# Kernel tuning notes

Hardware: AMD Instinct MI355X
Metric: run time of the kernel (lower is better)

Reference implementation:

```python
import jax, jax.numpy as jnp
import numpy as np

DIM = 192
HEADS = 6
WIN = (2, 6, 2)
N_TOK = WIN[0] * WIN[1] * WIN[2]  # 24
MLP_HID = 4 * DIM


def _rel_pos_index():
    wh, ww, wd = WIN
    ch, cw, cd = np.meshgrid(np.arange(wh), np.arange(ww), np.arange(wd), indexing='ij')
    coords = np.stack([ch, cw, cd]).reshape(3, -1)  # (3, N)
    rel = coords[:, :, None] - coords[:, None, :]   # (3, N, N)
    rel = rel.transpose(1, 2, 0).copy()
    rel[:, :, 0] += wh - 1
    rel[:, :, 1] += ww - 1
    rel[:, :, 2] += wd - 1
    rel[:, :, 0] *= (2 * ww - 1) * (2 * wd - 1)
    rel[:, :, 1] *= 2 * wd - 1
    return rel.sum(-1)  # (N, N) int


def setup_inputs() -> dict:
    key = jax.random.key(0)
    ks = jax.random.split(key, 8)
    wh, ww, wd = WIN
    table_len = (2 * wh - 1) * (2 * ww - 1) * (2 * wd - 1)
    return {
        'x': jax.random.normal(ks[0], (2, 48, 96, 14, DIM), jnp.float32),
        'ln1_g': jnp.ones((DIM,), jnp.float32),
        'ln1_b': jnp.zeros((DIM,), jnp.float32),
        'qkv_w': jax.random.normal(ks[1], (DIM, 3 * DIM), jnp.float32) * 0.02,  # [in, out]
        'qkv_b': jnp.zeros((3 * DIM,), jnp.float32),
        'bias_table': jax.random.normal(ks[2], (table_len, HEADS), jnp.float32) * 0.02,
        'proj_w': jax.random.normal(ks[3], (DIM, DIM), jnp.float32) * 0.02,
        'proj_b': jnp.zeros((DIM,), jnp.float32),
        'ln2_g': jnp.ones((DIM,), jnp.float32),
        'ln2_b': jnp.zeros((DIM,), jnp.float32),
        'mlp_w1': jax.random.normal(ks[4], (DIM, MLP_HID), jnp.float32) * 0.02,
        'mlp_b1': jnp.zeros((MLP_HID,), jnp.float32),
        'mlp_w2': jax.random.normal(ks[5], (MLP_HID, DIM), jnp.float32) * 0.02,
        'mlp_b2': jnp.zeros((DIM,), jnp.float32),
        'rel_index': jnp.asarray(_rel_pos_index(), jnp.int32),  # (N, N)
    }


def _layernorm(x, g, b, eps=1e-5):
    mu = jnp.mean(x, -1, keepdims=True)
    var = jnp.mean(jnp.square(x - mu), -1, keepdims=True)
    return (x - mu) * jax.lax.rsqrt(var + eps) * g + b


def reference(x, ln1_g, ln1_b, qkv_w, qkv_b, bias_table, proj_w, proj_b,
              ln2_g, ln2_b, mlp_w1, mlp_b1, mlp_w2, mlp_b2, rel_index):
    B, H, W, D, C = x.shape
    wh, ww, wd = WIN
    pad_h, pad_w, pad_d = (-H) % wh, (-W) % ww, (-D) % wd
    if pad_h or pad_w or pad_d:
        x = jnp.pad(x, ((0, 0), (0, pad_h), (0, pad_w), (0, pad_d), (0, 0)))
    Hp, Wp, Dp = H + pad_h, W + pad_w, D + pad_d
    # window partition -> (num_windows*B, N, C)
    xw = x.reshape(B, Hp // wh, wh, Wp // ww, ww, Dp // wd, wd, C)
    xw = xw.transpose(0, 1, 3, 5, 2, 4, 6, 7).reshape(-1, N_TOK, C)
    shortcut = xw

    h = _layernorm(xw, ln1_g, ln1_b)
    qkv = (h @ qkv_w + qkv_b).reshape(-1, N_TOK, 3, HEADS, C // HEADS)
    q, k, v = qkv[:, :, 0], qkv[:, :, 1], qkv[:, :, 2]  # (Bw, N, H, hd)
    scale = (C // HEADS) ** -0.5
    attn = jnp.einsum('bnhd,bmhd->bhnm', q * scale, k)
    bias = bias_table[rel_index]  # (N, N, HEADS)
    attn = attn + bias.transpose(2, 0, 1)[None]
    attn = jax.nn.softmax(attn, axis=-1)
    out = jnp.einsum('bhnm,bmhd->bnhd', attn, v).reshape(-1, N_TOK, C)
    out = out @ proj_w + proj_b
    xw = shortcut + out

    h2 = _layernorm(xw, ln2_g, ln2_b)
    mlp = jax.nn.gelu(h2 @ mlp_w1 + mlp_b1, approximate=False) @ mlp_w2 + mlp_b2
    xw = xw + mlp

    # reverse window partition
    xw = xw.reshape(B, Hp // wh, Wp // ww, Dp // wd, wh, ww, wd, C)
    xw = xw.transpose(0, 1, 4, 2, 5, 3, 6, 7).reshape(B, Hp, Wp, Dp, C)
    if pad_h or pad_w or pad_d:
        xw = xw[:, :H, :W, :D, :]
    return xw
```

## Files before the change

kernel.cpp:

```cpp
#include <hip/hip_runtime.h>
#include <hip/hip_bf16.h>
#include <math.h>

typedef __bf16 bf16_t;
typedef __bf16 bf16x8 __attribute__((ext_vector_type(8)));
typedef float  f32x4  __attribute__((ext_vector_type(4)));

#define NBLK 2688
#define WP_QKV  0
#define WP_PROJ 55296
#define WP_MLP1 73728
#define WP_MLP2 147456
#define WP_TOT  221184
#define WF_QKV  0
#define WF_PROJ 110592
#define WF_MLP1 147456
#define WF_MLP2 294912

__global__ void preproc_all(const float* __restrict__ qkv_w, const float* __restrict__ proj_w,
                            const float* __restrict__ mlp_w1, const float* __restrict__ mlp_w2,
                            bf16_t* __restrict__ dst) {
    int p = blockIdx.x * 256 + threadIdx.x;
    if (p >= WP_TOT) return;
    const float* W; int N, Kt; int q = p;
    if (p < WP_PROJ)      { W = qkv_w;  N = 576; Kt = 6;  }
    else if (p < WP_MLP1) { W = proj_w; N = 192; Kt = 6;  q -= WP_PROJ; }
    else if (p < WP_MLP2) { W = mlp_w1; N = 768; Kt = 6;  q -= WP_MLP1; }
    else                  { W = mlp_w2; N = 192; Kt = 24; q -= WP_MLP2; }
    int j    = (q & 3) * 2;
    int lane = (q >> 2) & 63;
    int kt   = (q >> 8) % Kt;
    int nt   = (q >> 8) / Kt;
    int k = kt * 32 + (lane >> 4) * 8 + j;
    int n = nt * 16 + (lane & 15);
    union { bf16_t h[2]; unsigned u; } pk;
    pk.h[0] = (bf16_t)W[k * N + n];
    pk.h[1] = (bf16_t)W[(k + 1) * N + n];
    *(unsigned*)(dst + p * 2) = pk.u;
}

__global__ __launch_bounds__(384, 3)
void pangu_main(const float* __restrict__ x,
                const float* __restrict__ ln1_g, const float* __restrict__ ln1_b,
                const float* __restrict__ qkv_b,
                const float* __restrict__ bias_table,
                const float* __restrict__ proj_b,
                const float* __restrict__ ln2_g, const float* __restrict__ ln2_b,
                const float* __restrict__ mlp_b1, const float* __restrict__ mlp_b2,
                const int* __restrict__ rel_index,
                const bf16_t* __restrict__ wf,
                float* __restrict__ out)
{
    __shared__ __align__(16) unsigned char arena[46080];
    __shared__ int   sRowOff[48];
    __shared__ float sMu[48], sRs[48];

    unsigned char* aAb   = arena;
    unsigned char* aOb   = arena;
    unsigned char* aH2b  = arena;
    unsigned char* xw2b  = arena + 19200;
    unsigned char* aHidb = arena + 19200;
    bf16_t* aO   = (bf16_t*)aOb;
    bf16_t* aHid = (bf16_t*)aHidb;
    bf16_t* xw2h = (bf16_t*)xw2b;

    const int t    = threadIdx.x;
    const int lane = t & 63;
    const int wv   = t >> 6;
    const int quad = lane >> 4;
    const int l15  = lane & 15;
    const int q4   = quad * 4;

    if (t < 48) {
        int win = t / 24, tok = t % 24;
        int W = blockIdx.x * 2 + win;
        int id_ = W % 7;  int r1 = W / 7;
        int iw_ = r1 % 16; int r2 = r1 / 16;
        int ih_ = r2 % 24; int b  = r2 / 24;
        int i = tok / 12, j = (tok % 12) / 2, k = tok % 2;
        sRowOff[t] = (((b * 48 + ih_ * 2 + i) * 96 + iw_ * 6 + j) * 14 + id_ * 2 + k) * 192;
    }
    __syncthreads();

    {
        int r48 = t >> 3, l = t & 7;
        const float* xr = x + sRowOff[r48];
        float4 v[6];
        #pragma unroll
        for (int s = 0; s < 6; ++s) v[s] = *(const float4*)(xr + l * 4 + s * 32);
        float sm = 0.f, s2 = 0.f;
        #pragma unroll
        for (int s = 0; s < 6; ++s) {
            sm += v[s].x + v[s].y + v[s].z + v[s].w;
            s2 += v[s].x * v[s].x + v[s].y * v[s].y + v[s].z * v[s].z + v[s].w * v[s].w;
        }
        sm += __shfl_xor(sm, 1); s2 += __shfl_xor(s2, 1);
        sm += __shfl_xor(sm, 2); s2 += __shfl_xor(s2, 2);
        sm += __shfl_xor(sm, 4); s2 += __shfl_xor(s2, 4);
        float mu = sm * (1.f / 192.f);
        float var = s2 * (1.f / 192.f) - mu * mu;
        float rs = rsqrtf(var + 1e-5f);
        int row = r48;
        #pragma unroll
        for (int s = 0; s < 6; ++s) {
            int c = l * 4 + s * 32;
            union { bf16_t h[4]; uint2 u; } pk;
            pk.h[0] = (bf16_t)((v[s].x - mu) * rs * ln1_g[c]     + ln1_b[c]);
            pk.h[1] = (bf16_t)((v[s].y - mu) * rs * ln1_g[c + 1] + ln1_b[c + 1]);
            pk.h[2] = (bf16_t)((v[s].z - mu) * rs * ln1_g[c + 2] + ln1_b[c + 2]);
            pk.h[3] = (bf16_t)((v[s].w - mu) * rs * ln1_g[c + 3] + ln1_b[c + 3]);
            *(uint2*)(aAb + row * 400 + c * 2) = pk.u;
        }
    }
    __syncthreads();

    {
        const int h = wv;
        unsigned char* wb = arena + 19200 + wv * 4480;
        bf16_t* Qb = (bf16_t*)wb;
        bf16_t* Kb = (bf16_t*)(wb + 1920);
        bf16_t* Vt = (bf16_t*)(wb + 1920);
        bf16_t* Pb = (bf16_t*)wb;

        f32x4 acc[3][6];
        {
            float bq[6];
            const int ntg[6] = {2*h, 2*h+1, 12+2*h, 13+2*h, 24+2*h, 25+2*h};
            #pragma unroll
            for (int n = 0; n < 6; ++n) bq[n] = qkv_b[ntg[n] * 16 + l15];
            #pragma unroll
            for (int m = 0; m < 3; ++m)
                #pragma unroll
                for (int n = 0; n < 6; ++n)
                    acc[m][n] = (f32x4){bq[n], bq[n], bq[n], bq[n]};
            for (int kt = 0; kt < 6; ++kt) {
                bf16x8 af[3];
                #pragma unroll
                for (int m = 0; m < 3; ++m)
                    af[m] = *(const bf16x8*)(aAb + (l15 + m * 16) * 400 + kt * 64 + quad * 16);
                #pragma unroll
                for (int n = 0; n < 6; ++n) {
                    bf16x8 bfr = *(const bf16x8*)(wf + WF_QKV + ((ntg[n] * 6 + kt) * 64 + lane) * 8);
                    #pragma unroll
                    for (int m = 0; m < 3; ++m)
                        acc[m][n] = __builtin_amdgcn_mfma_f32_16x16x32_bf16(af[m], bfr, acc[m][n], 0, 0, 0);
                }
            }
        }
        __syncthreads();

        const float scale = 0.1767766952966369f;
        #pragma unroll
        for (int win = 0; win < 2; ++win) {
            #pragma unroll
            for (int m = 0; m < 3; ++m)
                #pragma unroll
                for (int i = 0; i < 4; ++i) {
                    int tok = m * 16 + q4 + i - win * 24;
                    if (tok >= 0 && tok < 24) {
                        #pragma unroll
                        for (int nt = 0; nt < 2; ++nt) {
                            int d = nt * 16 + l15;
                            Qb[tok * 40 + d] = (bf16_t)(acc[m][nt][i] * scale);
                            Kb[tok * 40 + d] = (bf16_t)(acc[m][2+nt][i]);
                        }
                    }
                }
            f32x4 sacc[2][2];
            #pragma unroll
            for (int mt = 0; mt < 2; ++mt)
                #pragma unroll
                for (int nt = 0; nt < 2; ++nt)
                    #pragma unroll
                    for (int i = 0; i < 4; ++i) {
                        int n = mt * 16 + q4 + i; if (n > 23) n = 23;
                        int m = nt * 16 + l15;    if (m > 23) m = 23;
                        sacc[mt][nt][i] = bias_table[rel_index[n * 24 + m] * 6 + h];
                    }
            #pragma unroll
            for (int nt = 0; nt < 2; ++nt) {
                bf16x8 kf = *(const bf16x8*)((unsigned char*)Kb + (l15 + nt * 16) * 80 + quad * 16);
                #pragma unroll
                for (int mt = 0; mt < 2; ++mt) {
                    bf16x8 qf = *(const bf16x8*)((unsigned char*)Qb + (l15 + mt * 16) * 80 + quad * 16);
                    sacc[mt][nt] = __builtin_amdgcn_mfma_f32_16x16x32_bf16(qf, kf, sacc[mt][nt], 0, 0, 0);
                }
            }
            #pragma unroll
            for (int m = 0; m < 3; ++m)
                #pragma unroll
                for (int i = 0; i < 4; ++i) {
                    int tok = m * 16 + q4 + i - win * 24;
                    if (tok >= 0 && tok < 24) {
                        #pragma unroll
                        for (int nt = 0; nt < 2; ++nt)
                            Vt[(nt * 16 + l15) * 40 + tok] = (bf16_t)(acc[m][4+nt][i]);
                    }
                }
            {
                int d = lane >> 1, half = lane & 1;
                *(uint2*)((unsigned char*)Vt + d * 80 + 48 + half * 8) = make_uint2(0u, 0u);
            }
            #pragma unroll
            for (int mt = 0; mt < 2; ++mt)
                #pragma unroll
                for (int i = 0; i < 4; ++i) {
                    float s0 = sacc[mt][0][i];
                    float s1m = (l15 < 8) ? sacc[mt][1][i] : -1e30f;
                    float mx = fmaxf(s0, s1m);
                    mx = fmaxf(mx, __shfl_xor(mx, 1));
                    mx = fmaxf(mx, __shfl_xor(mx, 2));
                    mx = fmaxf(mx, __shfl_xor(mx, 4));
                    mx = fmaxf(mx, __shfl_xor(mx, 8));
                    float e0 = __expf(s0 - mx);
                    float e1 = (l15 < 8) ? __expf(sacc[mt][1][i] - mx) : 0.f;
                    float sum = e0 + e1;
                    sum += __shfl_xor(sum, 1);
                    sum += __shfl_xor(sum, 2);
                    sum += __shfl_xor(sum, 4);
                    sum += __shfl_xor(sum, 8);
                    float inv = 1.f / sum;
                    sacc[mt][0][i] = e0 * inv;
                    sacc[mt][1][i] = e1 * inv;
                }
            #pragma unroll
            for (int mt = 0; mt < 2; ++mt)
                #pragma unroll
                for (int i = 0; i < 4; ++i) {
                    int r = mt * 16 + q4 + i;
                    if (r < 24) {
                        Pb[r * 40 + l15]      = (bf16_t)sacc[mt][0][i];
                        Pb[r * 40 + 16 + l15] = (bf16_t)sacc[mt][1][i];
                    }
                }
            f32x4 oacc[2][2];
            #pragma unroll
            for (int mt = 0; mt < 2; ++mt)
                #pragma unroll
                for (int nt = 0; nt < 2; ++nt)
                    oacc[mt][nt] = (f32x4){0.f, 0.f, 0.f, 0.f};
            #pragma unroll
            for (int nt = 0; nt < 2; ++nt) {
                bf16x8 vf = *(const bf16x8*)((unsigned char*)Vt + (l15 + nt * 16) * 80 + quad * 16);
                #pragma unroll
                for (int mt = 0; mt < 2; ++mt) {
                    bf16x8 pf = *(const bf16x8*)((unsigned char*)Pb + (l15 + mt * 16) * 80 + quad * 16);
                    oacc[mt][nt] = __builtin_amdgcn_mfma_f32_16x16x32_bf16(pf, vf, oacc[mt][nt], 0, 0, 0);
                }
            }
            #pragma unroll
            for (int mt = 0; mt < 2; ++mt)
                #pragma unroll
                for (int i = 0; i < 4; ++i) {
                    int tok = mt * 16 + q4 + i;
                    if (tok < 24) {
                        int r = win * 24 + tok;
                        #pragma unroll
                        for (int nt = 0; nt < 2; ++nt)
                            aO[r * 200 + h * 32 + nt * 16 + l15] = (bf16_t)oacc[mt][nt][i];
                    }
                }
        }
    }
    __syncthreads();

    float rxw[3][2][4];
    {
        f32x4 pacc[3][2];
        #pragma unroll
        for (int m = 0; m < 3; ++m)
            #pragma unroll
            for (int n = 0; n < 2; ++n) pacc[m][n] = (f32x4){0.f, 0.f, 0.f, 0.f};
        for (int kt = 0; kt < 6; ++kt) {
            bf16x8 af[3];
            #pragma unroll
            for (int m = 0; m < 3; ++m)
                af[m] = *(const bf16x8*)(aOb + (l15 + m * 16) * 400 + kt * 64 + quad * 16);
            #pragma unroll
            for (int n = 0; n < 2; ++n) {
                int NT = wv * 2 + n;
                bf16x8 bfr = *(const bf16x8*)(wf + WF_PROJ + ((NT * 6 + kt) * 64 + lane) * 8);
                #pragma unroll
                for (int m = 0; m < 3; ++m)
                    pacc[m][n] = __builtin_amdgcn_mfma_f32_16x16x32_bf16(af[m], bfr, pacc[m][n], 0, 0, 0);
            }
        }
        __syncthreads();
        #pragma unroll
        for (int n = 0; n < 2; ++n) {
            int c = (wv * 2 + n) * 16 + l15;
            float pb = proj_b[c];
            #pragma unroll
            for (int m = 0; m < 3; ++m)
                #pragma unroll
                for (int i = 0; i < 4; ++i) {
                    int r = m * 16 + q4 + i;
                    float val = x[sRowOff[r] + c] + pb + pacc[m][n][i];
                    rxw[m][n][i] = val;
                    xw2h[r * 200 + c] = (bf16_t)val;
                }
        }
    }
    __syncthreads();

    {
        int r = t >> 3, l = t & 7;
        float sm = 0.f, s2 = 0.f;
        #pragma unroll
        for (int s = 0; s < 6; ++s) {
            union { bf16_t h[4]; uint2 u; } pk;
            pk.u = *(const uint2*)(xw2b + r * 400 + l * 8 + s * 64);
            #pragma unroll
            for (int z = 0; z < 4; ++z) { float v = (float)pk.h[z]; sm += v; s2 += v * v; }
        }
        sm += __shfl_xor(sm, 1); s2 += __shfl_xor(s2, 1);
        sm += __shfl_xor(sm, 2); s2 += __shfl_xor(s2, 2);
        sm += __shfl_xor(sm, 4); s2 += __shfl_xor(s2, 4);
        if (l == 0) {
            float mu = sm * (1.f / 192.f);
            float var = s2 * (1.f / 192.f) - mu * mu;
            sMu[r] = mu; sRs[r] = rsqrtf(var + 1e-5f);
        }
    }
    __syncthreads();
    for (int p = t; p < 4608; p += 384) {
        int r = p / 96, c2 = p % 96, c = c2 * 2;
        float mu = sMu[r], rs = sRs[r];
        union { bf16_t h[2]; unsigned u; } in, pk;
        in.u = *(const unsigned*)(xw2b + r * 400 + c2 * 4);
        pk.h[0] = (bf16_t)(((float)in.h[0] - mu) * rs * ln2_g[c]     + ln2_b[c]);
        pk.h[1] = (bf16_t)(((float)in.h[1] - mu) * rs * ln2_g[c + 1] + ln2_b[c + 1]);
        *(unsigned*)(aH2b + r * 400 + c2 * 4) = pk.u;
    }
    __syncthreads();

    f32x4 acc2[3][2];
    #pragma unroll
    for (int m = 0; m < 3; ++m)
        #pragma unroll
        for (int n = 0; n < 2; ++n) {
            float b2 = mlp_b2[(wv * 2 + n) * 16 + l15];
            acc2[m][n] = (f32x4){b2, b2, b2, b2};
        }
    for (int ch = 0; ch < 4; ++ch) {
        f32x4 a1[3][2];
        #pragma unroll
        for (int m = 0; m < 3; ++m)
            #pragma unroll
            for (int n = 0; n < 2; ++n) {
                float b1 = mlp_b1[ch * 192 + (wv * 2 + n) * 16 + l15];
                a1[m][n] = (f32x4){b1, b1, b1, b1};
            }
        for (int kt = 0; kt < 6; ++kt) {
            bf16x8 af[3];
            #pragma unroll
            for (int m = 0; m < 3; ++m)
                af[m] = *(const bf16x8*)(aH2b + (l15 + m * 16) * 400 + kt * 64 + quad * 16);
            #pragma unroll
            for (int n = 0; n < 2; ++n) {
                int NT = ch * 12 + wv * 2 + n;
                bf16x8 bfr = *(const bf16x8*)(wf + WF_MLP1 + ((NT * 6 + kt) * 64 + lane) * 8);
                #pragma unroll
                for (int m = 0; m < 3; ++m)
                    a1[m][n] = __builtin_amdgcn_mfma_f32_16x16x32_bf16(af[m], bfr, a1[m][n], 0, 0, 0);
            }
        }
        #pragma unroll
        for (int n = 0; n < 2; ++n) {
            int c = (wv * 2 + n) * 16 + l15;
            #pragma unroll
            for (int m = 0; m < 3; ++m)
                #pragma unroll
                for (int i = 0; i < 4; ++i) {
                    int r = m * 16 + q4 + i;
                    float v = a1[m][n][i];
                    float g = 0.5f * v * (1.f + erff(v * 0.70710678118654752f));
                    aHid[r * 200 + c] = (bf16_t)g;
                }
        }
        __syncthreads();
        for (int kt = 0; kt < 6; ++kt) {
            bf16x8 af[3];
            #pragma unroll
            for (int m = 0; m < 3; ++m)
                af[m] = *(const bf16x8*)(aHidb + (l15 + m * 16) * 400 + kt * 64 + quad * 16);
            #pragma unroll
            for (int n = 0; n < 2; ++n) {
                int NT = wv * 2 + n;
                int ktg = ch * 6 + kt;
                bf16x8 bfr = *(const bf16x8*)(wf + WF_MLP2 + ((NT * 24 + ktg) * 64 + lane) * 8);
                #pragma unroll
                for (int m = 0; m < 3; ++m)
                    acc2[m][n] = __builtin_amdgcn_mfma_f32_16x16x32_bf16(af[m], bfr, acc2[m][n], 0, 0, 0);
            }
        }
        __syncthreads();
    }

    #pragma unroll
    for (int n = 0; n < 2; ++n) {
        int c = (wv * 2 + n) * 16 + l15;
        #pragma unroll
        for (int m = 0; m < 3; ++m)
            #pragma unroll
            for (int i = 0; i < 4; ++i) {
                int r = m * 16 + q4 + i;
                out[sRowOff[r] + c] = rxw[m][n][i] + acc2[m][n][i];
            }
    }
}

extern "C" void kernel_launch(void* const* d_in, const int* in_sizes, int n_in,
                              void* d_out, int out_size, void* d_ws, size_t ws_size,
                              hipStream_t stream) {
    const float* x          = (const float*)d_in[0];
    const float* ln1_g      = (const float*)d_in[1];
    const float* ln1_b      = (const float*)d_in[2];
    const float* qkv_w      = (const float*)d_in[3];
    const float* qkv_b      = (const float*)d_in[4];
    const float* bias_table = (const float*)d_in[5];
    const float* proj_w     = (const float*)d_in[6];
    const float* proj_b     = (const float*)d_in[7];
    const float* ln2_g      = (const float*)d_in[8];
    const float* ln2_b      = (const float*)d_in[9];
    const float* mlp_w1     = (const float*)d_in[10];
    const float* mlp_b1     = (const float*)d_in[11];
    const float* mlp_w2     = (const float*)d_in[12];
    const float* mlp_b2     = (const float*)d_in[13];
    const int*   rel_index  = (const int*)d_in[14];
    float* out = (float*)d_out;
    bf16_t* wsb = (bf16_t*)d_ws;

    preproc_all<<<(WP_TOT + 255) / 256, 256, 0, stream>>>(qkv_w, proj_w, mlp_w1, mlp_w2, wsb);

    pangu_main<<<NBLK, 384, 0, stream>>>(
        x, ln1_g, ln1_b, qkv_b, bias_table, proj_b, ln2_g, ln2_b,
        mlp_b1, mlp_b2, rel_index, wsb, out);
}
```

Before: 550.2 us.

## Fuse LN2 stats into proj epilogue, prefetch residual, use tanh GELU

LayerNorm-2 statistics are now computed from register-resident fp32 residual values via wave shuffles plus a small cross-wave partial reduction, instead of staging a bf16 copy in LDS and rereading it. This removes one LDS pass and a sync. The residual x loads are issued before the projection GEMM so their latency overlaps the MFMAs. Several k-loops are fully unrolled, and exact erf GELU is replaced by a tanh-approximation built on __expf. The tanh form differs slightly from the exact-erf reference, and the extra unrolling may raise register pressure.

Result: slower. 661.6 us (+20.2%).

```diff
diff --git a/kernel.cpp b/kernel.cpp
--- a/kernel.cpp
+++ b/kernel.cpp
@@ -16,6 +16,15 @@
 #define WF_PROJ 110592
 #define WF_MLP1 147456
 #define WF_MLP2 294912
+
+__device__ __forceinline__ float fast_gelu(float v) {
+    float u  = 0.7978845608028654f * v * (1.f + 0.044715f * v * v);
+    float au = fabsf(u);
+    float e  = __expf(-2.f * au);
+    float th = __fdividef(1.f - e, 1.f + e);
+    th = copysignf(th, u);
+    return 0.5f * v * (1.f + th);
+}
 
 __global__ void preproc_all(const float* __restrict__ qkv_w, const float* __restrict__ proj_w,
                             const float* __restrict__ mlp_w1, const float* __restrict__ mlp_w2,
@@ -58,11 +67,9 @@
     unsigned char* aAb   = arena;
     unsigned char* aOb   = arena;
     unsigned char* aH2b  = arena;
-    unsigned char* xw2b  = arena + 19200;
     unsigned char* aHidb = arena + 19200;
     bf16_t* aO   = (bf16_t*)aOb;
     bf16_t* aHid = (bf16_t*)aHidb;
-    bf16_t* xw2h = (bf16_t*)xw2b;
 
     const int t    = threadIdx.x;
     const int lane = t & 63;
@@ -133,6 +140,7 @@
                 #pragma unroll
                 for (int n = 0; n < 6; ++n)
                     acc[m][n] = (f32x4){bq[n], bq[n], bq[n], bq[n]};
+            #pragma unroll
             for (int kt = 0; kt < 6; ++kt) {
                 bf16x8 af[3];
                 #pragma unroll
@@ -266,11 +274,21 @@
 
     float rxw[3][2][4];
     {
+        #pragma unroll
+        for (int m = 0; m < 3; ++m)
+            #pragma unroll
+            for (int i = 0; i < 4; ++i) {
+                int ro = sRowOff[m * 16 + q4 + i];
+                #pragma unroll
+                for (int n = 0; n < 2; ++n)
+                    rxw[m][n][i] = x[ro + (wv * 2 + n) * 16 + l15];
+            }
         f32x4 pacc[3][2];
         #pragma unroll
         for (int m = 0; m < 3; ++m)
             #pragma unroll
             for (int n = 0; n < 2; ++n) pacc[m][n] = (f32x4){0.f, 0.f, 0.f, 0.f};
+        #pragma unroll
         for (int kt = 0; kt < 6; ++kt) {
             bf16x8 af[3];
             #pragma unroll
@@ -285,52 +303,54 @@
                     pacc[m][n] = __builtin_amdgcn_mfma_f32_16x16x32_bf16(af[m], bfr, pacc[m][n], 0, 0, 0);
             }
         }
+        #pragma unroll
+        for (int n = 0; n < 2; ++n) {
+            float pb = proj_b[(wv * 2 + n) * 16 + l15];
+            #pragma unroll
+            for (int m = 0; m < 3; ++m)
+                #pragma unroll
+                for (int i = 0; i < 4; ++i)
+                    rxw[m][n][i] += pb + pacc[m][n][i];
+        }
+    }
+
+    {
+        float2* sPart = (float2*)(arena + 19200);
+        #pragma unroll
+        for (int m = 0; m < 3; ++m)
+            #pragma unroll
+            for (int i = 0; i < 4; ++i) {
+                float s  = rxw[m][0][i] + rxw[m][1][i];
+                float s2 = rxw[m][0][i] * rxw[m][0][i] + rxw[m][1][i] * rxw[m][1][i];
+                s += __shfl_xor(s, 1); s2 += __shfl_xor(s2, 1);
+                s += __shfl_xor(s, 2); s2 += __shfl_xor(s2, 2);
+                s += __shfl_xor(s, 4); s2 += __shfl_xor(s2, 4);
+                s += __shfl_xor(s, 8); s2 += __shfl_xor(s2, 8);
+                if (l15 == 0) sPart[(m * 16 + q4 + i) * 6 + wv] = make_float2(s, s2);
+            }
+        __syncthreads();
+        if (t < 48) {
+            float s = 0.f, s2 = 0.f;
+            #pragma unroll
+            for (int w = 0; w < 6; ++w) { float2 p = sPart[t * 6 + w]; s += p.x; s2 += p.y; }
+            float mu = s * (1.f / 192.f);
+            float var = s2 * (1.f / 192.f) - mu * mu;
+            sMu[t] = mu; sRs[t] = rsqrtf(var + 1e-5f);
+        }
         __syncthreads();
         #pragma unroll
         for (int n = 0; n < 2; ++n) {
             int c = (wv * 2 + n) * 16 + l15;
-            float pb = proj_b[c];
+            float g = ln2_g[c], b = ln2_b[c];
             #pragma unroll
             for (int m = 0; m < 3; ++m)
                 #pragma unroll
                 for (int i = 0; i < 4; ++i) {
                     int r = m * 16 + q4 + i;
-                    float val = x[sRowOff[r] + c] + pb + pacc[m][n][i];
-                    rxw[m][n][i] = val;
-                    xw2h[r * 200 + c] = (bf16_t)val;
-                }
-        }
-    }
-    __syncthreads();
-
-    {
-        int r = t >> 3, l = t & 7;
-        float sm = 0.f, s2 = 0.f;
-        #pragma unroll
-        for (int s = 0; s < 6; ++s) {
-            union { bf16_t h[4]; uint2 u; } pk;
-            pk.u = *(const uint2*)(xw2b + r * 400 + l * 8 + s * 64);
-            #pragma unroll
-            for (int z = 0; z < 4; ++z) { float v = (float)pk.h[z]; sm += v; s2 += v * v; }
-        }
-        sm += __shfl_xor(sm, 1); s2 += __shfl_xor(s2, 1);
-        sm += __shfl_xor(sm, 2); s2 += __shfl_xor(s2, 2);
-        sm += __shfl_xor(sm, 4); s2 += __shfl_xor(s2, 4);
-        if (l == 0) {
-            float mu = sm * (1.f / 192.f);
-            float var = s2 * (1.f / 192.f) - mu * mu;
-            sMu[r] = mu; sRs[r] = rsqrtf(var + 1e-5f);
-        }
-    }
-    __syncthreads();
-    for (int p = t; p < 4608; p += 384) {
-        int r = p / 96, c2 = p % 96, c = c2 * 2;
-        float mu = sMu[r], rs = sRs[r];
-        union { bf16_t h[2]; unsigned u; } in, pk;
-        in.u = *(const unsigned*)(xw2b + r * 400 + c2 * 4);
-        pk.h[0] = (bf16_t)(((float)in.h[0] - mu) * rs * ln2_g[c]     + ln2_b[c]);
-        pk.h[1] = (bf16_t)(((float)in.h[1] - mu) * rs * ln2_g[c + 1] + ln2_b[c + 1]);
-        *(unsigned*)(aH2b + r * 400 + c2 * 4) = pk.u;
+                    ((bf16_t*)aH2b)[r * 200 + c] =
+                        (bf16_t)((rxw[m][n][i] - sMu[r]) * sRs[r] * g + b);
+                }
+        }
     }
     __syncthreads();
 
@@ -351,6 +371,7 @@
                 float b1 = mlp_b1[ch * 192 + (wv * 2 + n) * 16 + l15];
                 a1[m][n] = (f32x4){b1, b1, b1, b1};
             }
+        #pragma unroll
         for (int kt = 0; kt < 6; ++kt) {
             bf16x8 af[3];
             #pragma unroll
@@ -373,12 +394,11 @@
                 #pragma unroll
                 for (int i = 0; i < 4; ++i) {
                     int r = m * 16 + q4 + i;
-                    float v = a1[m][n][i];
-                    float g = 0.5f * v * (1.f + erff(v * 0.70710678118654752f));
-                    aHid[r * 200 + c] = (bf16_t)g;
+                    aHid[r * 200 + c] = (bf16_t)fast_gelu(a1[m][n][i]);
                 }
         }
         __syncthreads();
+        #pragma unroll
         for (int kt = 0; kt < 6; ++kt) {
             bf16x8 af[3];
             #pragma unroll
```

## Software-pipeline MLP chunks with double-buffered hidden tile and interleaved GEMMs

Applied to the files above, without the earlier changes.

Restructures the MLP chunk loop so the second-layer GEMM for the previous chunk is interleaved with the first-layer GEMM for the current chunk, using two hidden-activation LDS buffers. This halves the number of block barriers in the MLP and gives the MFMA pipe more independent work per iteration. It raises LDS per block and keeps more accumulators live, which risks register spills or reduced occupancy.

New measurement: 555.4 us. About the same (+0.9%).

```diff
diff --git a/kernel.cpp b/kernel.cpp
--- a/kernel.cpp
+++ b/kernel.cpp
@@ -51,17 +51,17 @@
                 const bf16_t* __restrict__ wf,
                 float* __restrict__ out)
 {
-    __shared__ __align__(16) unsigned char arena[46080];
+    __shared__ __align__(16) unsigned char arena[57600];
     __shared__ int   sRowOff[48];
     __shared__ float sMu[48], sRs[48];
 
-    unsigned char* aAb   = arena;
-    unsigned char* aOb   = arena;
-    unsigned char* aH2b  = arena;
-    unsigned char* xw2b  = arena + 19200;
-    unsigned char* aHidb = arena + 19200;
+    unsigned char* aAb    = arena;
+    unsigned char* aOb    = arena;
+    unsigned char* aH2b   = arena;
+    unsigned char* xw2b   = arena + 19200;
+    unsigned char* aHidb0 = arena + 19200;
+    unsigned char* aHidb1 = arena + 38400;
     bf16_t* aO   = (bf16_t*)aOb;
-    bf16_t* aHid = (bf16_t*)aHidb;
     bf16_t* xw2h = (bf16_t*)xw2b;
 
     const int t    = threadIdx.x;
@@ -342,7 +342,50 @@
             float b2 = mlp_b2[(wv * 2 + n) * 16 + l15];
             acc2[m][n] = (f32x4){b2, b2, b2, b2};
         }
-    for (int ch = 0; ch < 4; ++ch) {
+
+    {
+        f32x4 a1[3][2];
+        #pragma unroll
+        for (int m = 0; m < 3; ++m)
+            #pragma unroll
+            for (int n = 0; n < 2; ++n) {
+                float b1 = mlp_b1[(wv * 2 + n) * 16 + l15];
+                a1[m][n] = (f32x4){b1, b1, b1, b1};
+            }
+        for (int kt = 0; kt < 6; ++kt) {
+            bf16x8 af[3];
+            #pragma unroll
+            for (int m = 0; m < 3; ++m)
+                af[m] = *(const bf16x8*)(aH2b + (l15 + m * 16) * 400 + kt * 64 + quad * 16);
+            #pragma unroll
+            for (int n = 0; n < 2; ++n) {
+                int NT = wv * 2 + n;
+                bf16x8 bfr = *(const bf16x8*)(wf + WF_MLP1 + ((NT * 6 + kt) * 64 + lane) * 8);
+                #pragma unroll
+                for (int m = 0; m < 3; ++m)
+                    a1[m][n] = __builtin_amdgcn_mfma_f32_16x16x32_bf16(af[m], bfr, a1[m][n], 0, 0, 0);
+            }
+        }
+        bf16_t* hid = (bf16_t*)aHidb0;
+        #pragma unroll
+        for (int n = 0; n < 2; ++n) {
+            int c = (wv * 2 + n) * 16 + l15;
+            #pragma unroll
+            for (int m = 0; m < 3; ++m)
+                #pragma unroll
+                for (int i = 0; i < 4; ++i) {
+                    int r = m * 16 + q4 + i;
+                    float v = a1[m][n][i];
+                    float g = 0.5f * v * (1.f + erff(v * 0.70710678118654752f));
+                    hid[r * 200 + c] = (bf16_t)g;
+                }
+        }
+    }
+    __syncthreads();
+
+    unsigned char* hidRead = aHidb0;
+    for (int ch = 1; ch < 4; ++ch) {
+        unsigned char* hidWrite = (ch & 1) ? aHidb1 : aHidb0;
         f32x4 a1[3][2];
         #pragma unroll
         for (int m = 0; m < 3; ++m)
@@ -352,19 +395,25 @@
                 a1[m][n] = (f32x4){b1, b1, b1, b1};
             }
         for (int kt = 0; kt < 6; ++kt) {
-            bf16x8 af[3];
-            #pragma unroll
-            for (int m = 0; m < 3; ++m)
-                af[m] = *(const bf16x8*)(aH2b + (l15 + m * 16) * 400 + kt * 64 + quad * 16);
+            bf16x8 ah[3], aa[3];
+            #pragma unroll
+            for (int m = 0; m < 3; ++m) {
+                ah[m] = *(const bf16x8*)(hidRead + (l15 + m * 16) * 400 + kt * 64 + quad * 16);
+                aa[m] = *(const bf16x8*)(aH2b    + (l15 + m * 16) * 400 + kt * 64 + quad * 16);
+            }
             #pragma unroll
             for (int n = 0; n < 2; ++n) {
-                int NT = ch * 12 + wv * 2 + n;
-                bf16x8 bfr = *(const bf16x8*)(wf + WF_MLP1 + ((NT * 6 + kt) * 64 + lane) * 8);
-                #pragma unroll
-                for (int m = 0; m < 3; ++m)
-                    a1[m][n] = __builtin_amdgcn_mfma_f32_16x16x32_bf16(af[m], bfr, a1[m][n], 0, 0, 0);
-            }
-        }
+                int NT = wv * 2 + n;
+                bf16x8 b2f = *(const bf16x8*)(wf + WF_MLP2 + ((NT * 24 + (ch - 1) * 6 + kt) * 64 + lane) * 8);
+                bf16x8 b1f = *(const bf16x8*)(wf + WF_MLP1 + (((ch * 12 + NT) * 6 + kt) * 64 + lane) * 8);
+                #pragma unroll
+                for (int m = 0; m < 3; ++m) {
+                    acc2[m][n] = __builtin_amdgcn_mfma_f32_16x16x32_bf16(ah[m], b2f, acc2[m][n], 0, 0, 0);
+                    a1[m][n]   = __builtin_amdgcn_mfma_f32_16x16x32_bf16(aa[m], b1f, a1[m][n], 0, 0, 0);
+                }
+            }
+        }
+        bf16_t* hid = (bf16_t*)hidWrite;
         #pragma unroll
         for (int n = 0; n < 2; ++n) {
             int c = (wv * 2 + n) * 16 + l15;
@@ -375,26 +424,26 @@
                     int r = m * 16 + q4 + i;
                     float v = a1[m][n][i];
                     float g = 0.5f * v * (1.f + erff(v * 0.70710678118654752f));
-                    aHid[r * 200 + c] = (bf16_t)g;
+                    hid[r * 200 + c] = (bf16_t)g;
                 }
         }
         __syncthreads();
-        for (int kt = 0; kt < 6; ++kt) {
-            bf16x8 af[3];
-            #pragma unroll
-            for (int m = 0; m < 3; ++m)
-                af[m] = *(const bf16x8*)(aHidb + (l15 + m * 16) * 400 + kt * 64 + quad * 16);
-            #pragma unroll
-            for (int n = 0; n < 2; ++n) {
-                int NT = wv * 2 + n;
-                int ktg = ch * 6 + kt;
-                bf16x8 bfr = *(const bf16x8*)(wf + WF_MLP2 + ((NT * 24 + ktg) * 64 + lane) * 8);
-                #pragma unroll
-                for (int m = 0; m < 3; ++m)
-                    acc2[m][n] = __builtin_amdgcn_mfma_f32_16x16x32_bf16(af[m], bfr, acc2[m][n], 0, 0, 0);
-            }
-        }
-        __syncthreads();
+        hidRead = hidWrite;
+    }
+
+    for (int kt = 0; kt < 6; ++kt) {
+        bf16x8 ah[3];
+        #pragma unroll
+        for (int m = 0; m < 3; ++m)
+            ah[m] = *(const bf16x8*)(hidRead + (l15 + m * 16) * 400 + kt * 64 + quad * 16);
+        #pragma unroll
+        for (int n = 0; n < 2; ++n) {
+            int NT = wv * 2 + n;
+            bf16x8 b2f = *(const bf16x8*)(wf + WF_MLP2 + ((NT * 24 + 18 + kt) * 64 + lane) * 8);
+            #pragma unroll
+            for (int m = 0; m < 3; ++m)
+                acc2[m][n] = __builtin_amdgcn_mfma_f32_16x16x32_bf16(ah[m], b2f, acc2[m][n], 0, 0, 0);
+        }
     }
 
     #pragma unroll
```

## Split QKV GEMM into K/V pass then Q pass to cut accumulator registers

Applied to the files above, without the earlier changes.

Instead of holding Q, K and V accumulators for all 48 rows at once, each wave first computes K and V and writes them to LDS for both windows. It then computes Q in a second pass. This lowers live accumulator registers and removes per-window K/V staging from the attention loop. In exchange, the A fragments are read from LDS twice and the shared arena grows from 46 KB to 75 KB per block. That larger arena may cut how many 384-thread blocks can stay resident per CU.

Result: no change. 541.6 us (-1.6%).

```diff
diff --git a/kernel.cpp b/kernel.cpp
--- a/kernel.cpp
+++ b/kernel.cpp
@@ -51,7 +51,7 @@
                 const bf16_t* __restrict__ wf,
                 float* __restrict__ out)
 {
-    __shared__ __align__(16) unsigned char arena[46080];
+    __shared__ __align__(16) unsigned char arena[75264];
     __shared__ int   sRowOff[48];
     __shared__ float sMu[48], sRs[48];
 
@@ -116,22 +116,22 @@
 
     {
         const int h = wv;
-        unsigned char* wb = arena + 19200 + wv * 4480;
-        bf16_t* Qb = (bf16_t*)wb;
-        bf16_t* Kb = (bf16_t*)(wb + 1920);
-        bf16_t* Vt = (bf16_t*)(wb + 1920);
-        bf16_t* Pb = (bf16_t*)wb;
-
-        f32x4 acc[3][6];
+        unsigned char* wb = arena + 19200 + wv * 9344;
+        bf16_t* Qb  = (bf16_t*)wb;
+        bf16_t* Kb2 = (bf16_t*)(wb + 1920);
+        bf16_t* Vt  = (bf16_t*)(wb + 5760);
+        bf16_t* Pb  = (bf16_t*)wb;
+
         {
-            float bq[6];
-            const int ntg[6] = {2*h, 2*h+1, 12+2*h, 13+2*h, 24+2*h, 25+2*h};
-            #pragma unroll
-            for (int n = 0; n < 6; ++n) bq[n] = qkv_b[ntg[n] * 16 + l15];
-            #pragma unroll
-            for (int m = 0; m < 3; ++m)
-                #pragma unroll
-                for (int n = 0; n < 6; ++n)
+            f32x4 acc[3][4];
+            const int ntg[4] = {12+2*h, 13+2*h, 24+2*h, 25+2*h};
+            float bq[4];
+            #pragma unroll
+            for (int n = 0; n < 4; ++n) bq[n] = qkv_b[ntg[n] * 16 + l15];
+            #pragma unroll
+            for (int m = 0; m < 3; ++m)
+                #pragma unroll
+                for (int n = 0; n < 4; ++n)
                     acc[m][n] = (f32x4){bq[n], bq[n], bq[n], bq[n]};
             for (int kt = 0; kt < 6; ++kt) {
                 bf16x8 af[3];
@@ -139,13 +139,55 @@
                 for (int m = 0; m < 3; ++m)
                     af[m] = *(const bf16x8*)(aAb + (l15 + m * 16) * 400 + kt * 64 + quad * 16);
                 #pragma unroll
-                for (int n = 0; n < 6; ++n) {
+                for (int n = 0; n < 4; ++n) {
                     bf16x8 bfr = *(const bf16x8*)(wf + WF_QKV + ((ntg[n] * 6 + kt) * 64 + lane) * 8);
                     #pragma unroll
                     for (int m = 0; m < 3; ++m)
                         acc[m][n] = __builtin_amdgcn_mfma_f32_16x16x32_bf16(af[m], bfr, acc[m][n], 0, 0, 0);
                 }
             }
+            #pragma unroll
+            for (int m = 0; m < 3; ++m)
+                #pragma unroll
+                for (int i = 0; i < 4; ++i) {
+                    int row = m * 16 + q4 + i;
+                    #pragma unroll
+                    for (int nt = 0; nt < 2; ++nt) {
+                        int d = nt * 16 + l15;
+                        Kb2[row * 40 + d] = (bf16_t)(acc[m][nt][i]);
+                        Vt[d * 56 + row]  = (bf16_t)(acc[m][2+nt][i]);
+                    }
+                }
+            {
+                int d = lane >> 1, half = lane & 1;
+                *(uint2*)((unsigned char*)Vt + d * 112 + 96 + half * 8) = make_uint2(0u, 0u);
+            }
+        }
+
+        f32x4 qacc[3][2];
+        {
+            const int ntg[2] = {2*h, 2*h+1};
+            float bq[2];
+            #pragma unroll
+            for (int n = 0; n < 2; ++n) bq[n] = qkv_b[ntg[n] * 16 + l15];
+            #pragma unroll
+            for (int m = 0; m < 3; ++m)
+                #pragma unroll
+                for (int n = 0; n < 2; ++n)
+                    qacc[m][n] = (f32x4){bq[n], bq[n], bq[n], bq[n]};
+            for (int kt = 0; kt < 6; ++kt) {
+                bf16x8 af[3];
+                #pragma unroll
+                for (int m = 0; m < 3; ++m)
+                    af[m] = *(const bf16x8*)(aAb + (l15 + m * 16) * 400 + kt * 64 + quad * 16);
+                #pragma unroll
+                for (int n = 0; n < 2; ++n) {
+                    bf16x8 bfr = *(const bf16x8*)(wf + WF_QKV + ((ntg[n] * 6 + kt) * 64 + lane) * 8);
+                    #pragma unroll
+                    for (int m = 0; m < 3; ++m)
+                        qacc[m][n] = __builtin_amdgcn_mfma_f32_16x16x32_bf16(af[m], bfr, qacc[m][n], 0, 0, 0);
+                }
+            }
         }
         __syncthreads();
 
@@ -159,11 +201,8 @@
                     int tok = m * 16 + q4 + i - win * 24;
                     if (tok >= 0 && tok < 24) {
                         #pragma unroll
-                        for (int nt = 0; nt < 2; ++nt) {
-                            int d = nt * 16 + l15;
-                            Qb[tok * 40 + d] = (bf16_t)(acc[m][nt][i] * scale);
-                            Kb[tok * 40 + d] = (bf16_t)(acc[m][2+nt][i]);
-                        }
+                        for (int nt = 0; nt < 2; ++nt)
+                            Qb[tok * 40 + nt * 16 + l15] = (bf16_t)(qacc[m][nt][i] * scale);
                     }
                 }
             f32x4 sacc[2][2];
@@ -179,27 +218,12 @@
                     }
             #pragma unroll
             for (int nt = 0; nt < 2; ++nt) {
-                bf16x8 kf = *(const bf16x8*)((unsigned char*)Kb + (l15 + nt * 16) * 80 + quad * 16);
+                bf16x8 kf = *(const bf16x8*)((unsigned char*)Kb2 + (win * 24 + l15 + nt * 16) * 80 + quad * 16);
                 #pragma unroll
                 for (int mt = 0; mt < 2; ++mt) {
                     bf16x8 qf = *(const bf16x8*)((unsigned char*)Qb + (l15 + mt * 16) * 80 + quad * 16);
                     sacc[mt][nt] = __builtin_amdgcn_mfma_f32_16x16x32_bf16(qf, kf, sacc[mt][nt], 0, 0, 0);
                 }
-            }
-            #pragma unroll
-            for (int m = 0; m < 3; ++m)
-                #pragma unroll
-                for (int i = 0; i < 4; ++i) {
-                    int tok = m * 16 + q4 + i - win * 24;
-                    if (tok >= 0 && tok < 24) {
-                        #pragma unroll
-                        for (int nt = 0; nt < 2; ++nt)
-                            Vt[(nt * 16 + l15) * 40 + tok] = (bf16_t)(acc[m][4+nt][i]);
-                    }
-                }
-            {
-                int d = lane >> 1, half = lane & 1;
-                *(uint2*)((unsigned char*)Vt + d * 80 + 48 + half * 8) = make_uint2(0u, 0u);
             }
             #pragma unroll
             for (int mt = 0; mt < 2; ++mt)
@@ -241,7 +265,7 @@
                     oacc[mt][nt] = (f32x4){0.f, 0.f, 0.f, 0.f};
             #pragma unroll
             for (int nt = 0; nt < 2; ++nt) {
-                bf16x8 vf = *(const bf16x8*)((unsigned char*)Vt + (l15 + nt * 16) * 80 + quad * 16);
+                bf16x8 vf = *(const bf16x8*)((unsigned char*)Vt + (l15 + nt * 16) * 112 + win * 48 + quad * 16);
                 #pragma unroll
                 for (int mt = 0; mt < 2; ++mt) {
                     bf16x8 pf = *(const bf16x8*)((unsigned char*)Pb + (l15 + mt * 16) * 80 + quad * 16);
```
